# Kernel tuning notes

Measured on AMD Instinct MI355X. Metric: run time of the kernel, lower is better.

The kernel has to match this reference:

```python
import jax, jax.numpy as jnp
import numpy as np

H, W = 4096, 4096
KH, KW = 11, 11


def setup_inputs() -> dict:
    key = jax.random.key(0)
    k1, k2 = jax.random.split(key)
    x = jax.random.normal(k1, (H, W), dtype=jnp.float32)
    weight = jax.random.uniform(k2, (KH, KW), dtype=jnp.float32)
    bias = jnp.zeros((1,), dtype=jnp.float32)
    return {"x": x, "weight": weight, "bias": bias}


def reference(x, weight, bias):
    # corr2d: valid 2D cross-correlation of a single-channel image with a
    # single kernel, then add scalar bias. Output shape [H-KH+1, W-KW+1].
    out = jax.lax.conv_general_dilated(
        x[None, None, :, :],            # NCHW, N=C=1
        weight[None, None, :, :],       # OIHW, O=I=1
        window_strides=(1, 1),
        padding="VALID",
        dimension_numbers=("NCHW", "OIHW", "NCHW"),
    )[0, 0]
    return out + bias[0]
```

## Files before the change

### kernel.cpp

```cpp
#include <hip/hip_runtime.h>
#include <hip/hip_bf16.h>

#define IH 4096
#define IW 4096
#define KH 11
#define KW 11
#define OH (IH - KH + 1)
#define OW (IW - KW + 1)

#define BM 64
#define BN 64
#define TROWS   74
#define TSTRIDE 84
#define NC4     20
#define NCHUNK  (TROWS * NC4)
#define NITER   6
#define TILE_SHORTS (TROWS * TSTRIDE)
#define BMAT_SHORTS (KH * 512)

#define TILES_X 64
#define NTILE   4096

typedef short bf16x4 __attribute__((ext_vector_type(4)));
typedef short bf16x8 __attribute__((ext_vector_type(8)));
typedef float f32x4  __attribute__((ext_vector_type(4)));

__device__ __forceinline__ short f2b(float f) {
    __hip_bfloat16 h = __float2bfloat16(f);
    return __builtin_bit_cast(short, h);
}

__global__ void build_bmat(const float* __restrict__ w, short* __restrict__ bm) {
    const int tid = threadIdx.x;
#pragma unroll
    for (int t = 0; t < 22; ++t) {
        const int idx = tid + t * 256;
        const int kh = idx >> 9;
        const int j  = (idx >> 5) & 15;
        const int k  = idx & 31;
        const int d  = k - j;
        const float val = (d >= 0 && d < KW) ? w[kh * KW + d] : 0.f;
        bm[idx] = f2b(val);
    }
}

__device__ __forceinline__ void loadA(bf16x8 a[4], const short* __restrict__ ap) {
#pragma unroll
    for (int c = 0; c < 4; ++c) {
        bf16x4 lo = *reinterpret_cast<const bf16x4*>(ap + c * 16);
        bf16x4 hi = *reinterpret_cast<const bf16x4*>(ap + c * 16 + 4);
        a[c] = __builtin_shufflevector(lo, hi, 0, 1, 2, 3, 4, 5, 6, 7);
    }
}

__device__ __forceinline__ void mfma4(f32x4 acc[4], const bf16x8 a[4], bf16x8 b) {
#pragma unroll
    for (int c = 0; c < 4; ++c) {
        acc[c] = __builtin_amdgcn_mfma_f32_16x16x32_bf16(a[c], b, acc[c], 0, 0, 0);
    }
}

__global__ __launch_bounds__(256)
void conv2d_tlp(const float* __restrict__ x,
                const short* __restrict__ bg,
                const float* __restrict__ bias,
                float* __restrict__ out) {
    __shared__ short lds[TILE_SHORTS + BMAT_SHORTS];

    const int tid = threadIdx.x;
    const int blk = (blockIdx.x & 7) * (NTILE / 8) + (blockIdx.x >> 3);
    const int gy0 = (blk >> 6) * BM;
    const int gx0 = (blk & (TILES_X - 1)) * BN;

    const int lane = tid & 63;
    const int wv   = tid >> 6;
    const int g    = lane >> 4;
    const int li   = lane & 15;
    const float bv = bias[0];

#pragma unroll
    for (int it = 0; it < NITER; ++it) {
        const int i = tid + it * 256;
        if (i < NCHUNK) {
            const int r  = i / NC4;
            const int c4 = i - r * NC4;
            const int gy = gy0 + r;
            const int gx = gx0 + c4 * 4;
            float4 v = make_float4(0.f, 0.f, 0.f, 0.f);
            if (gy < IH && gx + 3 < IW) {
                v = *reinterpret_cast<const float4*>(x + (size_t)gy * IW + gx);
            }
            bf16x4 b = { f2b(v.x), f2b(v.y), f2b(v.z), f2b(v.w) };
            *reinterpret_cast<bf16x4*>(&lds[r * TSTRIDE + c4 * 4]) = b;
        }
    }
#pragma unroll
    for (int t = 0; t < 3; ++t) {
        const int idx = tid + t * 256;
        if (idx < (BMAT_SHORTS * 2) / 16) {
            reinterpret_cast<int4*>(&lds[TILE_SHORTS])[idx] =
                reinterpret_cast<const int4*>(bg)[idx];
        }
    }
    __syncthreads();

    f32x4 acc[4] = {};
    const short* ap = &lds[(16 * wv + li) * TSTRIDE + g * 8];
    const short* bp = &lds[TILE_SHORTS + li * 32 + g * 8];

    bf16x8 Ae[4], Ao[4], Be, Bo;
    loadA(Ae, ap);
    Be = *reinterpret_cast<const bf16x8*>(bp);

#pragma unroll 1
    for (int kh2 = 0; kh2 < 5; ++kh2) {
        loadA(Ao, ap + TSTRIDE);
        Bo = *reinterpret_cast<const bf16x8*>(bp + 512);
        mfma4(acc, Ae, Be);
        ap += 2 * TSTRIDE;
        bp += 1024;
        loadA(Ae, ap);
        Be = *reinterpret_cast<const bf16x8*>(bp);
        mfma4(acc, Ao, Bo);
    }
    mfma4(acc, Ae, Be);

#pragma unroll
    for (int c = 0; c < 4; ++c) {
        const int ox = gx0 + c * 16 + li;
        if (ox < OW) {
#pragma unroll
            for (int r = 0; r < 4; ++r) {
                const int oy = gy0 + wv * 16 + g * 4 + r;
                if (oy < OH) {
                    out[(size_t)oy * OW + ox] = acc[c][r] + bv;
                }
            }
        }
    }
}

extern "C" void kernel_launch(void* const* d_in, const int* in_sizes, int n_in,
                              void* d_out, int out_size, void* d_ws, size_t ws_size,
                              hipStream_t stream) {
    const float* x    = (const float*)d_in[0];
    const float* w    = (const float*)d_in[1];
    const float* bias = (const float*)d_in[2];
    float* out        = (float*)d_out;
    short* bm         = (short*)d_ws;

    build_bmat<<<dim3(1), dim3(256), 0, stream>>>(w, bm);

    dim3 grid(NTILE);
    dim3 block(256);
    conv2d_tlp<<<grid, block, 0, stream>>>(x, bm, bias, out);
}
```

Before: 38.79 us.

## Stage input tile to LDS via direct global-to-LDS DMA, convert in compute loop

Global-to-LDS loads now bring the input tile straight into shared memory as fp32, bypassing registers, and the bf16 conversion moves into the A-operand loads inside the MFMA loop. The block grows to 512 threads (8 waves), with each wave computing half of a 16-row stripe (two 16-column MFMA tiles instead of four), which raises parallelism per tile. The goal is to cut staging latency and VGPR pressure. The cost is double the LDS footprint for the tile, repeated conversions of the same data across overlapping rows, and fewer MFMAs per wave to hide the latency.

```diff
diff --git a/kernel.cpp b/kernel.cpp
--- a/kernel.cpp
+++ b/kernel.cpp
@@ -11,17 +11,15 @@
 #define BM 64
 #define BN 64
 #define TROWS   74
-#define TSTRIDE 84
-#define NC4     20
-#define NCHUNK  (TROWS * NC4)
-#define NITER   6
-#define TILE_SHORTS (TROWS * TSTRIDE)
+#define FSTRIDE 84
+#define NCH_ROW 21
+#define NCHUNK  (TROWS * NCH_ROW)
+#define TILE_FLOATS (TROWS * FSTRIDE)
 #define BMAT_SHORTS (KH * 512)
 
 #define TILES_X 64
 #define NTILE   4096
 
-typedef short bf16x4 __attribute__((ext_vector_type(4)));
 typedef short bf16x8 __attribute__((ext_vector_type(8)));
 typedef float f32x4  __attribute__((ext_vector_type(4)));
 
@@ -44,28 +42,32 @@
     }
 }
 
-__device__ __forceinline__ void loadA(bf16x8 a[4], const short* __restrict__ ap) {
+__device__ __forceinline__ void loadA2cvt(bf16x8 a[2], const float* __restrict__ ap) {
 #pragma unroll
-    for (int c = 0; c < 4; ++c) {
-        bf16x4 lo = *reinterpret_cast<const bf16x4*>(ap + c * 16);
-        bf16x4 hi = *reinterpret_cast<const bf16x4*>(ap + c * 16 + 4);
-        a[c] = __builtin_shufflevector(lo, hi, 0, 1, 2, 3, 4, 5, 6, 7);
+    for (int c = 0; c < 2; ++c) {
+        f32x4 p = *reinterpret_cast<const f32x4*>(ap + c * 16);
+        f32x4 q = *reinterpret_cast<const f32x4*>(ap + c * 16 + 4);
+        bf16x8 v;
+#pragma unroll
+        for (int e = 0; e < 4; ++e) { v[e] = f2b(p[e]); v[4 + e] = f2b(q[e]); }
+        a[c] = v;
     }
 }
 
-__device__ __forceinline__ void mfma4(f32x4 acc[4], const bf16x8 a[4], bf16x8 b) {
+__device__ __forceinline__ void mfma2(f32x4 acc[2], const bf16x8 a[2], bf16x8 b) {
 #pragma unroll
-    for (int c = 0; c < 4; ++c) {
+    for (int c = 0; c < 2; ++c) {
         acc[c] = __builtin_amdgcn_mfma_f32_16x16x32_bf16(a[c], b, acc[c], 0, 0, 0);
     }
 }
 
-__global__ __launch_bounds__(256)
-void conv2d_tlp(const float* __restrict__ x,
+__global__ __launch_bounds__(512)
+void conv2d_dma(const float* __restrict__ x,
                 const short* __restrict__ bg,
                 const float* __restrict__ bias,
                 float* __restrict__ out) {
-    __shared__ short lds[TILE_SHORTS + BMAT_SHORTS];
+    __shared__ float tile[TILE_FLOATS];
+    __shared__ short bmat[BMAT_SHORTS];
 
     const int tid = threadIdx.x;
     const int blk = (blockIdx.x & 7) * (NTILE / 8) + (blockIdx.x >> 3);
@@ -73,65 +75,69 @@
     const int gx0 = (blk & (TILES_X - 1)) * BN;
 
     const int lane = tid & 63;
-    const int wv   = tid >> 6;
-    const int g    = lane >> 4;
-    const int li   = lane & 15;
-    const float bv = bias[0];
+    const int wvb  = tid & ~63;
 
 #pragma unroll
-    for (int it = 0; it < NITER; ++it) {
-        const int i = tid + it * 256;
+    for (int it = 0; it < 4; ++it) {
+        const int i = tid + it * 512;
         if (i < NCHUNK) {
-            const int r  = i / NC4;
-            const int c4 = i - r * NC4;
+            const int r  = i / NCH_ROW;
+            const int c4 = i - r * NCH_ROW;
             const int gy = gy0 + r;
             const int gx = gx0 + c4 * 4;
-            float4 v = make_float4(0.f, 0.f, 0.f, 0.f);
-            if (gy < IH && gx + 3 < IW) {
-                v = *reinterpret_cast<const float4*>(x + (size_t)gy * IW + gx);
-            }
-            bf16x4 b = { f2b(v.x), f2b(v.y), f2b(v.z), f2b(v.w) };
-            *reinterpret_cast<bf16x4*>(&lds[r * TSTRIDE + c4 * 4]) = b;
+            const float* src = (c4 < 20 && gy < IH && gx + 3 < IW)
+                               ? (x + (size_t)gy * IW + gx) : x;
+            __builtin_amdgcn_global_load_lds(
+                (const __attribute__((address_space(1))) void*)src,
+                (__attribute__((address_space(3))) void*)&tile[(it * 512 + wvb) * 4],
+                16, 0, 0);
         }
     }
 #pragma unroll
-    for (int t = 0; t < 3; ++t) {
-        const int idx = tid + t * 256;
+    for (int t = 0; t < 2; ++t) {
+        const int idx = tid + t * 512;
         if (idx < (BMAT_SHORTS * 2) / 16) {
-            reinterpret_cast<int4*>(&lds[TILE_SHORTS])[idx] =
+            reinterpret_cast<int4*>(bmat)[idx] =
                 reinterpret_cast<const int4*>(bg)[idx];
         }
     }
     __syncthreads();
 
-    f32x4 acc[4] = {};
-    const short* ap = &lds[(16 * wv + li) * TSTRIDE + g * 8];
-    const short* bp = &lds[TILE_SHORTS + li * 32 + g * 8];
+    const int wv = tid >> 6;
+    const int wr = wv >> 1;
+    const int ch = wv & 1;
+    const int g  = lane >> 4;
+    const int li = lane & 15;
+    const float bv = bias[0];
 
-    bf16x8 Ae[4], Ao[4], Be, Bo;
-    loadA(Ae, ap);
+    f32x4 acc[2] = {};
+    const float* ap = &tile[(16 * wr + li) * FSTRIDE + ch * 32 + g * 8];
+    const short* bp = &bmat[li * 32 + g * 8];
+
+    bf16x8 Ae[2], Ao[2], Be, Bo;
+    loadA2cvt(Ae, ap);
     Be = *reinterpret_cast<const bf16x8*>(bp);
 
 #pragma unroll 1
     for (int kh2 = 0; kh2 < 5; ++kh2) {
-        loadA(Ao, ap + TSTRIDE);
+        loadA2cvt(Ao, ap + FSTRIDE);
         Bo = *reinterpret_cast<const bf16x8*>(bp + 512);
-        mfma4(acc, Ae, Be);
-        ap += 2 * TSTRIDE;
+        mfma2(acc, Ae, Be);
+        ap += 2 * FSTRIDE;
         bp += 1024;
-        loadA(Ae, ap);
+        loadA2cvt(Ae, ap);
         Be = *reinterpret_cast<const bf16x8*>(bp);
-        mfma4(acc, Ao, Bo);
+        mfma2(acc, Ao, Bo);
     }
-    mfma4(acc, Ae, Be);
+    mfma2(acc, Ae, Be);
 
 #pragma unroll
-    for (int c = 0; c < 4; ++c) {
-        const int ox = gx0 + c * 16 + li;
+    for (int c = 0; c < 2; ++c) {
+        const int ox = gx0 + ch * 32 + c * 16 + li;
         if (ox < OW) {
 #pragma unroll
             for (int r = 0; r < 4; ++r) {
-                const int oy = gy0 + wv * 16 + g * 4 + r;
+                const int oy = gy0 + wr * 16 + g * 4 + r;
                 if (oy < OH) {
                     out[(size_t)oy * OW + ox] = acc[c][r] + bv;
                 }
@@ -152,6 +158,6 @@
     build_bmat<<<dim3(1), dim3(256), 0, stream>>>(w, bm);
 
     dim3 grid(NTILE);
-    dim3 block(256);
-    conv2d_tlp<<<grid, block, 0, stream>>>(x, bm, bias, out);
+    dim3 block(512);
+    conv2d_dma<<<grid, block, 0, stream>>>(x, bm, bias, out);
 }
```

After: 41.60 us. +7.2%, slower.
